# Kernel tuning notes

Measured on AMD Instinct MI355X. Metric: run time of the kernel, lower is better.

The kernel has to match this reference:

```python
import jax, jax.numpy as jnp
import numpy as np

N, E, B, H = 10000, 50000, 512, 64
IN_CH, EDGE_DIM = 11, 4
N_LAYERS, M_STEPS = 4, 3

silu = jax.nn.silu


def setup_inputs() -> dict:
    key = jax.random.key(0)
    ks = jax.random.split(key, 20)
    rn = lambda k, s, sc=0.1: jax.random.normal(k, s, jnp.float32) * sc
    w = 2 * H  # nn_width_factor * hidden
    inp = {
        "x": rn(ks[0], (N, IN_CH), 1.0),
        "edge_attr": jax.random.uniform(ks[1], (E, EDGE_DIM), jnp.float32),
        "pos": rn(ks[2], (N, 3), 1.0),
        "edge_index": jax.random.randint(ks[3], (2, E), 0, N),
        "batch": jnp.sort(jax.random.randint(ks[4], (N,), 0, B)),
        "fl_W": rn(ks[5], (H, IN_CH), 0.3), "fl_b": jnp.zeros(H),
        "nn_W1": rn(ks[6], (w, EDGE_DIM + 1), 0.3), "nn_b1": jnp.zeros(w),
        "nn_W2": rn(ks[7], (H * H, w), 0.02), "nn_b2": jnp.zeros(H * H),
        "root_W": rn(ks[8], (H, H)), "root_b": jnp.zeros(H),
        "gru_Wih": rn(ks[9], (3 * H, H)), "gru_Whh": rn(ks[10], (3 * H, H)),
        "gru_bih": jnp.zeros(3 * H), "gru_bhh": jnp.zeros(3 * H),
        "lstm_Wih": rn(ks[11], (4 * H, 2 * H)), "lstm_Whh": rn(ks[12], (4 * H, H)),
        "lstm_bih": jnp.zeros(4 * H), "lstm_bhh": jnp.zeros(4 * H),
        "out_W1": rn(ks[13], (H, 2 * H)), "out_b1": jnp.zeros(H),
        "out_W2": rn(ks[14], (1, H)), "out_b2": jnp.zeros(1),
    }
    return inp


def _fwd(x, edge_attr, pos, fl_W, fl_b, nn_W1, nn_b1, nn_W2, nn_b2,
         root_W, root_b, gru_Wih, gru_Whh, gru_bih, gru_bhh,
         lstm_Wih, lstm_Whh, lstm_bih, lstm_bhh,
         out_W1, out_b1, out_W2, out_b2, edge_index, batch):
    src, dst = edge_index[0], edge_index[1]
    x = silu(x @ fl_W.T + fl_b)          # [N, H]
    h = x                                 # GRU hidden state

    # Edge-conditioned weights (shared conv + fixed edge_attr/pos -> compute once)
    dist = jnp.linalg.norm(pos[src] - pos[dst], axis=-1, keepdims=True)  # [E,1]
    ef = jnp.concatenate([edge_attr, dist], axis=-1)                      # [E,5]
    W_edge = (silu(ef @ nn_W1.T + nn_b1) @ nn_W2.T + nn_b2).reshape(E, H, H)
    deg = jnp.clip(jax.ops.segment_sum(jnp.ones((E,), x.dtype), dst, num_segments=N), 1.0)[:, None]

    for _ in range(N_LAYERS):
        # NNConv message: x_j @ W(e_ij), mean-aggregated at target i
        m = jnp.einsum('ei,eio->eo', x[src], W_edge)                      # [E, H]
        agg = jax.ops.segment_sum(m, dst, num_segments=N) / deg
        xc = silu(x @ root_W.T + root_b + agg)
        # GRU cell (seq_len=1)
        gi = xc @ gru_Wih.T + gru_bih
        gh = h @ gru_Whh.T + gru_bhh
        i_r, i_z, i_n = jnp.split(gi, 3, axis=-1)
        h_r, h_z, h_n = jnp.split(gh, 3, axis=-1)
        r = jax.nn.sigmoid(i_r + h_r)
        z = jax.nn.sigmoid(i_z + h_z)
        n = jnp.tanh(i_n + r * h_n)
        x = (1.0 - z) * n + z * h
        h = x

    # Set2Set readout (M processing steps, LSTM over graphs)
    q_star = jnp.zeros((B, 2 * H), x.dtype)
    hl = jnp.zeros((B, H), x.dtype)
    cl = jnp.zeros((B, H), x.dtype)
    for _ in range(M_STEPS):
        g = q_star @ lstm_Wih.T + lstm_bih + hl @ lstm_Whh.T + lstm_bhh
        gi_, gf_, gg_, go_ = jnp.split(g, 4, axis=-1)
        cl = jax.nn.sigmoid(gf_) * cl + jax.nn.sigmoid(gi_) * jnp.tanh(gg_)
        hl = jax.nn.sigmoid(go_) * jnp.tanh(cl)
        e = jnp.sum(x * hl[batch], axis=-1)                               # [N]
        mmax = jax.ops.segment_max(e, batch, num_segments=B)
        a = jnp.exp(e - mmax[batch])
        a = a / jax.ops.segment_sum(a, batch, num_segments=B)[batch]
        r_read = jax.ops.segment_sum(a[:, None] * x, batch, num_segments=B)
        q_star = jnp.concatenate([hl, r_read], axis=-1)

    out = silu(q_star @ out_W1.T + out_b1) @ out_W2.T + out_b2            # [B,1]
    return out.squeeze(-1)


def reference(x, edge_index, edge_attr, pos, batch, fl_W, fl_b, nn_W1, nn_b1,
              nn_W2, nn_b2, root_W, root_b, gru_Wih, gru_Whh, gru_bih, gru_bhh,
              lstm_Wih, lstm_Whh, lstm_bih, lstm_bhh, out_W1, out_b1, out_W2, out_b2):
    return _fwd(x, edge_attr, pos, fl_W, fl_b, nn_W1, nn_b1, nn_W2, nn_b2,
                root_W, root_b, gru_Wih, gru_Whh, gru_bih, gru_bhh,
                lstm_Wih, lstm_Whh, lstm_bih, lstm_bhh,
                out_W1, out_b1, out_W2, out_b2, edge_index, batch)
```

## Files before the change

### kernel.cpp

```cpp
#include <hip/hip_runtime.h>
#include <stdint.h>


#define NN 10000
#define EE 50000
#define BBG 512

typedef __attribute__((ext_vector_type(8))) short short8;
typedef __attribute__((ext_vector_type(4))) float f32x4;
typedef __attribute__((ext_vector_type(2))) float f32x2;

__device__ __forceinline__ float b2f(unsigned short u) {
  return __uint_as_float(((unsigned)u) << 16);
}
__device__ __forceinline__ float b2f_lo(unsigned u) { return __uint_as_float(u << 16); }
__device__ __forceinline__ float b2f_hi(unsigned u) { return __uint_as_float(u & 0xFFFF0000u); }
__device__ __forceinline__ unsigned short f2b(float f) {
  unsigned u = __float_as_uint(f);
  u += 0x7FFFu + ((u >> 16) & 1u);
  return (unsigned short)(u >> 16);
}
__device__ __forceinline__ float sigm(float x) { return 1.0f / (1.0f + __expf(-x)); }
__device__ __forceinline__ float siluf(float x) { return x / (1.0f + __expf(-x)); }
__device__ __forceinline__ float rawf(const void* p, int f, int i) {
  return f ? b2f(((const unsigned short*)p)[i]) : ((const float*)p)[i];
}
__device__ __forceinline__ float rdlane(int v, int k) {
  return __int_as_float(__builtin_amdgcn_readlane(v, k));
}

__global__ __launch_bounds__(256) void k_detect(const unsigned* __restrict__ w,
                                                int* __restrict__ flag) {
  __shared__ int cnt;
  if (threadIdx.x == 0) cnt = 0;
  __syncthreads();
  int c = 0;
  for (int i = threadIdx.x; i < 4096; i += 256) {
    unsigned lo = w[i] & 0xFFFFu;
    if (lo - 0x3A00u < 0x600u) c++;
  }
  atomicAdd(&cnt, c);
  __syncthreads();
  if (threadIdx.x == 0) *flag = (cnt > 2048) ? 1 : 0;
}

#define NCVT 20
struct Cvt {
  const void* src[NCVT];
  float* dst[NCVT];
  int n[NCVT];
};

__global__ __launch_bounds__(256) void k_convert(Cvt c, const int* __restrict__ flag) {
  const int f = *flag;
  const int stride = gridDim.x * blockDim.x;
  const int tid = blockIdx.x * blockDim.x + threadIdx.x;
#pragma unroll 1
  for (int a = 0; a < NCVT; a++) {
    const int n = c.n[a];
    const float* sf = (const float*)c.src[a];
    const unsigned short* sb = (const unsigned short*)c.src[a];
    float* d = c.dst[a];
    for (int i = tid; i < n; i += stride) d[i] = f ? b2f(sb[i]) : sf[i];
  }
}

__global__ __launch_bounds__(256) void k_ltrans(const float* __restrict__ Wih,
                                                const float* __restrict__ Whh,
                                                const float* __restrict__ W1,
                                                const float* __restrict__ rW,
                                                const float* __restrict__ gWih,
                                                const float* __restrict__ gWhh,
                                                float* __restrict__ WihT,
                                                float* __restrict__ WhhT,
                                                float* __restrict__ W1T,
                                                float* __restrict__ rWT,
                                                float* __restrict__ gWihT,
                                                float* __restrict__ gWhhT) {
  int j = blockIdx.x * 256 + threadIdx.x;
  if (j < 32768) {
    int r = j & 255, k = j >> 8;
    WihT[k * 256 + r] = Wih[r * 128 + k];
  } else if (j < 49152) {
    int q = j - 32768;
    int r = q & 255, k = q >> 8;
    WhhT[k * 256 + r] = Whh[r * 64 + k];
  } else if (j < 57344) {
    int q = j - 49152;
    int o = q & 63, k = q >> 6;
    W1T[k * 64 + o] = W1[o * 128 + k];
  } else if (j < 61440) {
    int q = j - 57344;
    int o = q & 63, k = q >> 6;
    rWT[k * 64 + o] = rW[o * 64 + k];
  } else if (j < 73728) {
    int q = j - 61440;
    int r = q % 192, k = q / 192;
    gWihT[k * 192 + r] = gWih[r * 64 + k];
  } else if (j < 86016) {
    int q = j - 73728;
    int r = q % 192, k = q / 192;
    gWhhT[k * 192 + r] = gWhh[r * 64 + k];
  }
}

__global__ __launch_bounds__(256) void k_hist(const int* __restrict__ ei,
                                              int* __restrict__ cnt,
                                              int* __restrict__ cntd) {
  int e = blockIdx.x * 256 + threadIdx.x;
  if (e < EE) {
    atomicAdd(cnt + ei[e], 1);
    atomicAdd(cntd + ei[EE + e], 1);
  }
}

__global__ __launch_bounds__(256) void k_scan(const int* __restrict__ cnt,
                                              const int* __restrict__ cntd,
                                              int* __restrict__ eptr,
                                              int* __restrict__ cursor,
                                              float* __restrict__ invd) {
  __shared__ int part[256];
  const int t = threadIdx.x;
  const int c0 = t * 40;
  int s = 0;
  for (int i = 0; i < 40; i++) {
    int idx = c0 + i;
    if (idx < NN) s += cnt[idx];
  }
  part[t] = s;
  __syncthreads();
  if (t == 0) {
    int run = 0;
    for (int i = 0; i < 256; i++) { int v = part[i]; part[i] = run; run += v; }
  }
  __syncthreads();
  int run = part[t];
  for (int i = 0; i < 40; i++) {
    int idx = c0 + i;
    if (idx < NN) {
      eptr[idx] = run;
      cursor[idx] = run;
      run += cnt[idx];
      invd[idx] = 1.0f / fmaxf((float)cntd[idx], 1.0f);
    }
  }
  if (t == 255) eptr[NN] = EE;
}

__global__ __launch_bounds__(256) void k_scatter(const int* __restrict__ ei,
                                                 int* __restrict__ cursor,
                                                 int* __restrict__ eord) {
  int e = blockIdx.x * 256 + threadIdx.x;
  if (e < EE) {
    int pos = atomicAdd(cursor + ei[e], 1);
    eord[pos] = e;
  }
}

__global__ __launch_bounds__(256) void k_sperm(const unsigned short* __restrict__ s_bf,
                                               const int* __restrict__ ei,
                                               const int* __restrict__ eord,
                                               unsigned* __restrict__ s_srt,
                                               int* __restrict__ dst_srt) {
  const int j = blockIdx.x * 4 + (threadIdx.x >> 6);
  const int lane = threadIdx.x & 63;
  const int e = eord[j];
  s_srt[(size_t)j * 64 + lane] = ((const unsigned*)s_bf)[(size_t)e * 64 + lane];
  if (lane == 0) dst_srt[j] = ei[EE + e];
}

__global__ __launch_bounds__(256) void k_lift(const void* __restrict__ xin,
                                              const float* __restrict__ flW,
                                              const float* __restrict__ flb,
                                              const float* __restrict__ b2,
                                              float* __restrict__ x,
                                              unsigned short* __restrict__ xb,
                                              float* __restrict__ xb2,
                                              float* __restrict__ agg,
                                              const int* __restrict__ flag) {
  const int f = *flag;
  int node = blockIdx.x * 4 + (threadIdx.x >> 6);
  int h = threadIdx.x & 63;
  float acc = flb[h];
#pragma unroll
  for (int c = 0; c < 11; c++)
    acc += rawf(xin, f, node * 11 + c) * flW[h * 11 + c];
  float v = siluf(acc);
  x[node * 64 + h] = v;
  xb[node * 64 + h] = f2b(v);
  int xvi = __float_as_int(v);
  float a2 = 0.0f;
#pragma unroll 8
  for (int i = 0; i < 64; i++) {
    float xi = rdlane(xvi, i);
    a2 += xi * b2[i * 64 + h];
  }
  xb2[node * 64 + h] = a2;
  agg[(size_t)node * 64 + h] = 0.0f;
}

__global__ __launch_bounds__(256) void k_sdeg(const void* __restrict__ ea,
                                              const void* __restrict__ pos,
                                              const int* __restrict__ ei,
                                              const float* __restrict__ W1,
                                              const float* __restrict__ b1,
                                              unsigned short* __restrict__ s_bf,
                                              const int* __restrict__ flag) {
  const int f = *flag;
  int e = blockIdx.x * 2 + (threadIdx.x >> 7);
  int k = threadIdx.x & 127;
  int src = ei[e], dst = ei[EE + e];
  float dx = rawf(pos, f, src * 3 + 0) - rawf(pos, f, dst * 3 + 0);
  float dy = rawf(pos, f, src * 3 + 1) - rawf(pos, f, dst * 3 + 1);
  float dz = rawf(pos, f, src * 3 + 2) - rawf(pos, f, dst * 3 + 2);
  float dist = sqrtf(dx * dx + dy * dy + dz * dz);
  float acc = b1[k];
  acc += rawf(ea, f, e * 4 + 0) * W1[k * 5 + 0];
  acc += rawf(ea, f, e * 4 + 1) * W1[k * 5 + 1];
  acc += rawf(ea, f, e * 4 + 2) * W1[k * 5 + 2];
  acc += rawf(ea, f, e * 4 + 3) * W1[k * 5 + 3];
  acc += dist * W1[k * 5 + 4];
  s_bf[e * 128 + k] = f2b(siluf(acc));
}

__global__ __launch_bounds__(256) void k_w2t(const float* __restrict__ W2,
                                             unsigned short* __restrict__ W2t) {
  int j = blockIdx.x * 256 + threadIdx.x;
  int i = j & 63;
  int k = (j >> 6) & 127;
  int o = j >> 13;
  W2t[j] = f2b(W2[(size_t)(i * 64 + o) * 128 + k]);
}

template <int KC>
__global__ __launch_bounds__(256) void k_T(const unsigned short* __restrict__ xb,
                                           const unsigned short* __restrict__ W2t,
                                           unsigned short* __restrict__ Tc, int K0) {
  __shared__ unsigned short sh[2 * 128 * 72];
  unsigned short* As = sh;
  unsigned short* Bs = sh + 128 * 72;
  const int t = threadIdx.x;
  const int n0 = blockIdx.x * 128;
  const int c0 = blockIdx.y * 128;
  const int lane = t & 63;
  const int w = t >> 6;
  const int lm = lane & 15;
  const int quad = lane >> 4;
  const int wm = w & 1;
  const int wn = w >> 1;

  for (int p = t; p < 128 * 8; p += 256) {
    int r = p >> 3, cc = (p & 7) * 8;
    uint4 v = make_uint4(0u, 0u, 0u, 0u);
    if (n0 + r < NN) v = *reinterpret_cast<const uint4*>(xb + (size_t)(n0 + r) * 64 + cc);
    *reinterpret_cast<uint4*>(&As[r * 72 + cc]) = v;
  }
  for (int p = t; p < 128 * 8; p += 256) {
    int r = p >> 3, cc = (p & 7) * 8;
    int c = c0 + r;
    int o = c / KC;
    int kg = K0 + (c % KC);
    uint4 v = *reinterpret_cast<const uint4*>(W2t + (size_t)(o * 128 + kg) * 64 + cc);
    *reinterpret_cast<uint4*>(&Bs[r * 72 + cc]) = v;
  }
  __syncthreads();

  f32x4 acc[4][4];
#pragma unroll
  for (int mt = 0; mt < 4; mt++)
#pragma unroll
    for (int nt = 0; nt < 4; nt++) acc[mt][nt] = (f32x4)(0.0f);

#pragma unroll
  for (int ks = 0; ks < 2; ks++) {
    const int kk = ks * 32 + quad * 8;
    short8 af[4], bfr[4];
#pragma unroll
    for (int mt = 0; mt < 4; mt++)
      af[mt] = *reinterpret_cast<const short8*>(&As[(wm * 64 + mt * 16 + lm) * 72 + kk]);
#pragma unroll
    for (int nt = 0; nt < 4; nt++)
      bfr[nt] = *reinterpret_cast<const short8*>(&Bs[(wn * 64 + nt * 16 + lm) * 72 + kk]);
#pragma unroll
    for (int mt = 0; mt < 4; mt++)
#pragma unroll
      for (int nt = 0; nt < 4; nt++)
        acc[mt][nt] = __builtin_amdgcn_mfma_f32_16x16x32_bf16(af[mt], bfr[nt], acc[mt][nt], 0, 0, 0);
  }

  __syncthreads();
  unsigned short* st = sh;
#pragma unroll
  for (int nt = 0; nt < 4; nt++) {
    int col = wn * 64 + nt * 16 + lm;
#pragma unroll
    for (int mt = 0; mt < 4; mt++) {
#pragma unroll
      for (int reg = 0; reg < 4; reg++) {
        int row = wm * 64 + mt * 16 + quad * 4 + reg;
        st[row * 132 + col] = f2b(acc[mt][nt][reg]);
      }
    }
  }
  __syncthreads();
  const int r16 = t >> 4;
  const int c8 = (t & 15) * 8;
#pragma unroll
  for (int it = 0; it < 8; it++) {
    int row = it * 16 + r16;
    int n = n0 + row;
    if (n < NN) {
      uint2 v0 = *reinterpret_cast<const uint2*>(&st[row * 132 + c8]);
      uint2 v1 = *reinterpret_cast<const uint2*>(&st[row * 132 + c8 + 4]);
      uint4 v = make_uint4(v0.x, v0.y, v1.x, v1.y);
      *reinterpret_cast<uint4*>(Tc + (size_t)n * (64 * KC) + c0 + c8) = v;
    }
  }
}

__global__ __launch_bounds__(256) void k_group(const unsigned short* __restrict__ Tc,
                                               const unsigned* __restrict__ s_srt,
                                               const int* __restrict__ dst_srt,
                                               const float* __restrict__ xb2,
                                               const int* __restrict__ eptr,
                                               float* __restrict__ agg) {
  const int n = blockIdx.x * 4 + (threadIdx.x >> 6);
  const int lane = threadIdx.x & 63;
  const int beg = eptr[n], end = eptr[n + 1];
  if (beg == end) return;
  const int lm = lane & 15;
  const int quad = lane >> 4;

  short8 bf[4][4];
#pragma unroll
  for (int ks = 0; ks < 4; ks++)
#pragma unroll
    for (int ot = 0; ot < 4; ot++)
      bf[ks][ot] = *reinterpret_cast<const short8*>(
          Tc + (size_t)n * 8192 + (ot * 16 + lm) * 128 + ks * 32 + quad * 8);

  float xv[4];
#pragma unroll
  for (int ot = 0; ot < 4; ot++) xv[ot] = xb2[(size_t)n * 64 + ot * 16 + lm];

  for (int tile = beg; tile < end; tile += 16) {
    int eidx = tile + lm;
    if (eidx >= EE) eidx = EE - 1;
    f32x4 acc[4];
#pragma unroll
    for (int ot = 0; ot < 4; ot++) acc[ot] = (f32x4)(0.0f);
#pragma unroll
    for (int ks = 0; ks < 4; ks++) {
      short8 af = *reinterpret_cast<const short8*>(
          (const unsigned short*)s_srt + (size_t)eidx * 128 + ks * 32 + quad * 8);
#pragma unroll
      for (int ot = 0; ot < 4; ot++)
        acc[ot] = __builtin_amdgcn_mfma_f32_16x16x32_bf16(af, bf[ks][ot], acc[ot], 0, 0, 0);
    }
#pragma unroll
    for (int reg = 0; reg < 4; reg++) {
      int edge = tile + quad * 4 + reg;
      if (edge < end) {
        int dst = dst_srt[edge];
#pragma unroll
        for (int ot = 0; ot < 4; ot++)
          atomicAdd(agg + (size_t)dst * 64 + ot * 16 + lm, acc[ot][reg] + xv[ot]);
      }
    }
  }
}

template <int KC>
__global__ __launch_bounds__(256) void k_emsg(const unsigned short* __restrict__ Tc,
                                              const unsigned short* __restrict__ s_bf,
                                              const int* __restrict__ ei,
                                              float* __restrict__ m, int K0, int first) {
  int e = blockIdx.x * 4 + (threadIdx.x >> 6);
  int o = threadIdx.x & 63;
  int src = ei[e];
  const uint4* tv = reinterpret_cast<const uint4*>(Tc + ((size_t)src * 64 + o) * KC);
  const uint4* sv = reinterpret_cast<const uint4*>(s_bf + (size_t)e * 128 + K0);
  float acc = 0.0f;
#pragma unroll
  for (int j = 0; j < KC / 8; j++) {
    uint4 a = tv[j], b = sv[j];
    unsigned aa[4] = {a.x, a.y, a.z, a.w};
    unsigned bb[4] = {b.x, b.y, b.z, b.w};
#pragma unroll
    for (int q = 0; q < 4; q++)
      acc += b2f_lo(aa[q]) * b2f_lo(bb[q]) + b2f_hi(aa[q]) * b2f_hi(bb[q]);
  }
  float* mp = m + (size_t)e * 64 + o;
  if (first) *mp = acc;
  else *mp += acc;
}

__global__ __launch_bounds__(256) void k_aggm(const float* __restrict__ m,
                                              const float* __restrict__ xb2,
                                              const int* __restrict__ ei,
                                              float* __restrict__ agg) {
  int e = blockIdx.x * 4 + (threadIdx.x >> 6);
  int o = threadIdx.x & 63;
  int src = ei[e], dst = ei[EE + e];
  atomicAdd(agg + (size_t)dst * 64 + o, m[(size_t)e * 64 + o] + xb2[(size_t)src * 64 + o]);
}

__global__ __launch_bounds__(256) void k_xcgru(float* __restrict__ x,
                                               unsigned short* __restrict__ xb,
                                               float* __restrict__ agg,
                                               const float* __restrict__ invd,
                                               const float* __restrict__ rWT,
                                               const float* __restrict__ rb,
                                               const float* __restrict__ WihT,
                                               const float* __restrict__ WhhT,
                                               const float* __restrict__ bih,
                                               const float* __restrict__ bhh,
                                               const float* __restrict__ b2,
                                               float* __restrict__ xb2,
                                               int last) {
  const int node0 = (blockIdx.x * 4 + (threadIdx.x >> 6)) * 4;
  const int lane = threadIdx.x & 63;

  float xv[4], av[4], idv[4];
  int xvi[4];
#pragma unroll
  for (int nn = 0; nn < 4; nn++) {
    size_t base = (size_t)(node0 + nn) * 64 + lane;
    xv[nn] = x[base];
    av[nn] = agg[base];
    agg[base] = 0.0f;
    idv[nn] = invd[node0 + nn];
    xvi[nn] = __float_as_int(xv[nn]);
  }

  float acc[4] = {0, 0, 0, 0};
#pragma unroll 8
  for (int k = 0; k < 64; k++) {
    float rw = rWT[k * 64 + lane];
#pragma unroll
    for (int nn = 0; nn < 4; nn++) acc[nn] += rdlane(xvi[nn], k) * rw;
  }
  const float rbv = rb[lane];
  int xci[4];
#pragma unroll
  for (int nn = 0; nn < 4; nn++)
    xci[nn] = __float_as_int(siluf(acc[nn] + rbv + av[nn] * idv[nn]));

  float gi0[4], gi1[4], gi2[4], gh0[4], gh1[4], gh2[4];
  {
    const float bi0 = bih[lane], bi1 = bih[64 + lane], bi2 = bih[128 + lane];
    const float bh0 = bhh[lane], bh1 = bhh[64 + lane], bh2 = bhh[128 + lane];
#pragma unroll
    for (int nn = 0; nn < 4; nn++) {
      gi0[nn] = bi0; gi1[nn] = bi1; gi2[nn] = bi2;
      gh0[nn] = bh0; gh1[nn] = bh1; gh2[nn] = bh2;
    }
  }
#pragma unroll 2
  for (int k = 0; k < 64; k++) {
    const float* wi = WihT + k * 192;
    const float* wh = WhhT + k * 192;
    const float wi0 = wi[lane], wi1 = wi[64 + lane], wi2 = wi[128 + lane];
    const float wh0 = wh[lane], wh1 = wh[64 + lane], wh2 = wh[128 + lane];
#pragma unroll
    for (int nn = 0; nn < 4; nn++) {
      const float xck = rdlane(xci[nn], k);
      const float xvk = rdlane(xvi[nn], k);
      gi0[nn] += xck * wi0; gi1[nn] += xck * wi1; gi2[nn] += xck * wi2;
      gh0[nn] += xvk * wh0; gh1[nn] += xvk * wh1; gh2[nn] += xvk * wh2;
    }
  }

  int xni[4];
#pragma unroll
  for (int nn = 0; nn < 4; nn++) {
    const float r = sigm(gi0[nn] + gh0[nn]);
    const float z = sigm(gi1[nn] + gh1[nn]);
    const float ng = tanhf(gi2[nn] + r * gh2[nn]);
    const float xn = (1.0f - z) * ng + z * xv[nn];
    x[(size_t)(node0 + nn) * 64 + lane] = xn;
    xni[nn] = __float_as_int(xn);
  }

  if (!last) {
#pragma unroll
    for (int nn = 0; nn < 4; nn++)
      xb[(size_t)(node0 + nn) * 64 + lane] = f2b(__int_as_float(xni[nn]));
    float a2[4] = {0, 0, 0, 0};
#pragma unroll 8
    for (int i = 0; i < 64; i++) {
      const float bv = b2[i * 64 + lane];
#pragma unroll
      for (int nn = 0; nn < 4; nn++) a2[nn] += rdlane(xni[nn], i) * bv;
    }
#pragma unroll
    for (int nn = 0; nn < 4; nn++)
      xb2[(size_t)(node0 + nn) * 64 + lane] = a2[nn];
  }
}

__global__ __launch_bounds__(256) void k_s2s(const float* __restrict__ x,
                                             const int* __restrict__ batch,
                                             const float* __restrict__ WihT,
                                             const float* __restrict__ WhhT,
                                             const float* __restrict__ bih,
                                             const float* __restrict__ bhh,
                                             const float* __restrict__ W1T,
                                             const float* __restrict__ b1,
                                             const float* __restrict__ W2,
                                             const float* __restrict__ b2o,
                                             void* __restrict__ out,
                                             const int* __restrict__ flag) {
  const int b = blockIdx.x;
  const int t = threadIdx.x;
  const int lane = t & 63;
  const int w = t >> 6;
  int lo = 0, hi = NN;
  while (lo < hi) { int mid = (lo + hi) >> 1; if (batch[mid] < b) lo = mid + 1; else hi = mid; }
  const int ns = lo;
  hi = NN;
  while (lo < hi) { int mid = (lo + hi) >> 1; if (batch[mid] <= b) lo = mid + 1; else hi = mid; }
  const int cnt = lo - ns;

  __shared__ float hs[64], rs[64], cs[64], gs[256];
  __shared__ float es[512];
  __shared__ float red[4][64];
  __shared__ float wred[4], wsum[4];
  if (t < 64) { hs[t] = 0.0f; rs[t] = 0.0f; cs[t] = 0.0f; }
  __syncthreads();

  for (int step = 0; step < 3; step++) {
    float acc = bih[t] + bhh[t];
#pragma unroll 4
    for (int k = 0; k < 64; k++)
      acc += hs[k] * (WihT[k * 256 + t] + WhhT[k * 256 + t]);
#pragma unroll 4
    for (int k = 0; k < 64; k++)
      acc += rs[k] * WihT[(64 + k) * 256 + t];
    gs[t] = acc;
    __syncthreads();
    if (t < 64) {
      float ig = sigm(gs[t]), fg = sigm(gs[64 + t]);
      float gg = tanhf(gs[128 + t]), og = sigm(gs[192 + t]);
      float c = fg * cs[t] + ig * gg;
      cs[t] = c;
      hs[t] = og * tanhf(c);
    }
    __syncthreads();

    float mxw = -3.4e38f;
    for (int j = w; j < cnt; j += 4) {
      float v = x[(size_t)(ns + j) * 64 + lane] * hs[lane];
#pragma unroll
      for (int mm = 32; mm; mm >>= 1) v += __shfl_xor(v, mm, 64);
      if (lane == 0 && j < 512) es[j] = v;
      mxw = fmaxf(mxw, v);
    }
    if (lane == 0) wred[w] = mxw;
    __syncthreads();
    float mx = fmaxf(fmaxf(wred[0], wred[1]), fmaxf(wred[2], wred[3]));

    float ps = 0.0f;
    for (int i = t; i < cnt && i < 512; i += 256) {
      float a = __expf(es[i] - mx);
      es[i] = a;
      ps += a;
    }
#pragma unroll
    for (int mm = 32; mm; mm >>= 1) ps += __shfl_xor(ps, mm, 64);
    if (lane == 0) wsum[w] = ps;
    __syncthreads();
    float tot = wsum[0] + wsum[1] + wsum[2] + wsum[3];
    float inv = (cnt > 0) ? 1.0f / tot : 0.0f;

    float pr = 0.0f;
    for (int j = w; j < cnt && j < 512; j += 4)
      pr += es[j] * x[(size_t)(ns + j) * 64 + lane];
    red[w][lane] = pr;
    __syncthreads();
    if (t < 64)
      rs[t] = (red[0][t] + red[1][t] + red[2][t] + red[3][t]) * inv;
    __syncthreads();
  }

  if (t < 64) {
    float acc = b1[lane];
#pragma unroll 4
    for (int k = 0; k < 64; k++) acc += hs[k] * W1T[k * 64 + lane];
#pragma unroll 4
    for (int k = 0; k < 64; k++) acc += rs[k] * W1T[(64 + k) * 64 + lane];
    float u = siluf(acc) * W2[lane];
#pragma unroll
    for (int mm = 32; mm; mm >>= 1) u += __shfl_xor(u, mm, 64);
    if (lane == 0) {
      float v = u + b2o[0];
      if (*flag) ((unsigned short*)out)[b] = f2b(v);
      else ((float*)out)[b] = v;
    }
  }
}

template <int KC>
static void run_chunks(const unsigned short* xb, const unsigned short* W2t,
                       unsigned short* Tc, const unsigned short* s_bf,
                       const int* ei, float* m, hipStream_t stream) {
  const int nch = 128 / KC;
  for (int c = 0; c < nch; c++) {
    k_T<KC><<<dim3((NN + 127) / 128, (64 * KC) / 128), 256, 0, stream>>>(xb, W2t, Tc, c * KC);
    k_emsg<KC><<<EE / 4, 256, 0, stream>>>(Tc, s_bf, ei, m, c * KC, c == 0 ? 1 : 0);
  }
}

extern "C" void kernel_launch(void* const* d_in, const int* in_sizes, int n_in,
                              void* d_out, int out_size, void* d_ws, size_t ws_size,
                              hipStream_t stream) {
  (void)n_in; (void)out_size;
  const bool sig_order = (in_sizes[1] == 2 * EE);
  const void* p_x   = d_in[0];
  const void* p_ea  = sig_order ? d_in[2] : d_in[1];
  const void* p_pos = sig_order ? d_in[3] : d_in[2];
  const int* edge_index = (const int*)(sig_order ? d_in[1] : d_in[3]);
  const int* batch      = (const int*)d_in[4];
  const void* p_w[20];
  for (int i = 0; i < 20; i++) p_w[i] = d_in[5 + i];

  char* base = (char*)d_ws;
  size_t off = 0;
  auto alloc = [&](size_t bytes) -> char* {
    char* p = base + off;
    off = (off + bytes + 255) & ~(size_t)255;
    return p;
  };
  int* flag = (int*)alloc(4);
  static const int cvt_n[NCVT] = {
      64 * 11, 64, 128 * 5, 128, 4096 * 128, 4096,
      64 * 64, 64,
      192 * 64, 192 * 64, 192, 192,
      256 * 128, 256 * 64, 256, 256,
      64 * 128, 64, 64, 1};
  float* canon[NCVT];
  for (int i = 0; i < NCVT; i++) canon[i] = (float*)alloc((size_t)cvt_n[i] * 4);
  const float* c_flW  = canon[0];
  const float* c_flb  = canon[1];
  const float* c_W1   = canon[2];
  const float* c_b1   = canon[3];
  const float* c_W2   = canon[4];
  const float* c_b2   = canon[5];
  const float* c_rW   = canon[6];
  const float* c_rb   = canon[7];
  const float* c_gWih = canon[8];
  const float* c_gWhh = canon[9];
  const float* c_gbih = canon[10];
  const float* c_gbhh = canon[11];
  const float* c_lWih = canon[12];
  const float* c_lWhh = canon[13];
  const float* c_lbih = canon[14];
  const float* c_lbhh = canon[15];
  const float* c_oW1  = canon[16];
  const float* c_ob1  = canon[17];
  const float* c_oW2  = canon[18];
  const float* c_ob2  = canon[19];

  unsigned short* s_bf = (unsigned short*)alloc((size_t)EE * 128 * 2);
  unsigned* s_srt = (unsigned*)alloc((size_t)EE * 64 * 4 + 4096);
  int* dst_srt = (int*)alloc((size_t)EE * 4);
  float* m    = (float*)alloc((size_t)EE * 64 * 4);
  float* x    = (float*)alloc((size_t)NN * 64 * 4);
  unsigned short* xb = (unsigned short*)alloc((size_t)NN * 64 * 2);
  float* agg  = (float*)alloc((size_t)NN * 64 * 4);
  float* xb2  = (float*)alloc((size_t)NN * 64 * 4);
  unsigned short* W2t = (unsigned short*)alloc((size_t)4096 * 128 * 2);
  float* invd = (float*)alloc((size_t)NN * 4);
  int* cnt    = (int*)alloc((size_t)2 * NN * 4);
  int* cntd   = cnt + NN;
  int* eptr   = (int*)alloc((size_t)(NN + 1) * 4);
  int* cursor = (int*)alloc((size_t)NN * 4);
  int* eord   = (int*)alloc((size_t)EE * 4);
  float* WihT = (float*)alloc((size_t)128 * 256 * 4);
  float* WhhT = (float*)alloc((size_t)64 * 256 * 4);
  float* W1T  = (float*)alloc((size_t)128 * 64 * 4);
  float* rWT  = (float*)alloc((size_t)64 * 64 * 4);
  float* gWihT = (float*)alloc((size_t)64 * 192 * 4);
  float* gWhhT = (float*)alloc((size_t)64 * 192 * 4);
  size_t base_need = off;

  int KC = 0;
  const int kcs[5] = {128, 64, 32, 16, 8};
  for (int i = 0; i < 5; i++) {
    size_t need = base_need + (size_t)NN * 64 * kcs[i] * 2 + 256;
    if (need <= ws_size) { KC = kcs[i]; break; }
  }
  if (KC == 0) return;
  unsigned short* Tc = (unsigned short*)alloc((size_t)NN * 64 * KC * 2);

  k_detect<<<1, 256, 0, stream>>>((const unsigned*)p_ea, flag);
  Cvt cvt;
  for (int i = 0; i < 20; i++) cvt.src[i] = p_w[i];
  for (int i = 0; i < NCVT; i++) { cvt.dst[i] = canon[i]; cvt.n[i] = cvt_n[i]; }
  k_convert<<<512, 256, 0, stream>>>(cvt, flag);
  k_ltrans<<<336, 256, 0, stream>>>(c_lWih, c_lWhh, c_oW1, c_rW, c_gWih, c_gWhh,
                                    WihT, WhhT, W1T, rWT, gWihT, gWhhT);

  hipMemsetAsync(cnt, 0, (size_t)2 * NN * 4, stream);
  k_lift<<<NN / 4, 256, 0, stream>>>(p_x, c_flW, c_flb, c_b2, x, xb, xb2, agg, flag);
  k_sdeg<<<EE / 2, 256, 0, stream>>>(p_ea, p_pos, edge_index, c_W1, c_b1, s_bf, flag);
  k_w2t<<<(4096 * 128) / 256, 256, 0, stream>>>(c_W2, W2t);
  k_hist<<<(EE + 255) / 256, 256, 0, stream>>>(edge_index, cnt, cntd);
  k_scan<<<1, 256, 0, stream>>>(cnt, cntd, eptr, cursor, invd);
  k_scatter<<<(EE + 255) / 256, 256, 0, stream>>>(edge_index, cursor, eord);
  k_sperm<<<EE / 4, 256, 0, stream>>>(s_bf, edge_index, eord, s_srt, dst_srt);

  for (int layer = 0; layer < 4; layer++) {
    if (KC == 128) {
      k_T<128><<<dim3((NN + 127) / 128, 64), 256, 0, stream>>>(xb, W2t, Tc, 0);
      k_group<<<NN / 4, 256, 0, stream>>>(Tc, s_srt, dst_srt, xb2, eptr, agg);
    } else {
      switch (KC) {
        case 64: run_chunks<64>(xb, W2t, Tc, s_bf, edge_index, m, stream); break;
        case 32: run_chunks<32>(xb, W2t, Tc, s_bf, edge_index, m, stream); break;
        case 16: run_chunks<16>(xb, W2t, Tc, s_bf, edge_index, m, stream); break;
        default: run_chunks<8>(xb, W2t, Tc, s_bf, edge_index, m, stream); break;
      }
      k_aggm<<<EE / 4, 256, 0, stream>>>(m, xb2, edge_index, agg);
    }
    k_xcgru<<<NN / 16, 256, 0, stream>>>(x, xb, agg, invd, rWT, c_rb,
                                         gWihT, gWhhT, c_gbih, c_gbhh,
                                         c_b2, xb2, layer == 3 ? 1 : 0);
  }

  k_s2s<<<BBG, 256, 0, stream>>>(x, batch, WihT, WhhT, c_lbih, c_lbhh,
                                 W1T, c_ob1, c_oW2, c_ob2, d_out, flag);
}
```

Before: 655.3 us.

## Fuse per-node transform GEMM with edge gather-reduce, dropping the Tc buffer

Replaces the two-kernel path (k_T writes a 10000x8192 bf16 Tc tensor to global memory, then k_group reads it back and runs per-edge MFMAs) with one kernel, k_Tg. Each block computes a 128-node by 128-k tile of T for one output channel in shared memory, then walks the source-sorted edges of those nodes. For each edge it does a scalar bf16 dot product over 128 k and atomically adds the result into agg. This removes the large global round-trip of Tc and its allocation. In exchange, each edge's 256-byte s vector is re-read once per output channel (64 times), and MFMA edge math becomes scalar FMAs with one atomic per edge per channel.

Result: slower. 1.169 ms (+78.4%).

```diff
diff --git a/kernel.cpp b/kernel.cpp
--- a/kernel.cpp
+++ b/kernel.cpp
@@ -161,12 +161,16 @@
                                                const int* __restrict__ ei,
                                                const int* __restrict__ eord,
                                                unsigned* __restrict__ s_srt,
+                                               int* __restrict__ src_srt,
                                                int* __restrict__ dst_srt) {
   const int j = blockIdx.x * 4 + (threadIdx.x >> 6);
   const int lane = threadIdx.x & 63;
   const int e = eord[j];
   s_srt[(size_t)j * 64 + lane] = ((const unsigned*)s_bf)[(size_t)e * 64 + lane];
-  if (lane == 0) dst_srt[j] = ei[EE + e];
+  if (lane == 0) {
+    src_srt[j] = ei[e];
+    dst_srt[j] = ei[EE + e];
+  }
 }
 
 __global__ __launch_bounds__(256) void k_lift(const void* __restrict__ xin,
@@ -232,6 +236,106 @@
   W2t[j] = f2b(W2[(size_t)(i * 64 + o) * 128 + k]);
 }
 
+__global__ __launch_bounds__(256) void k_Tg(const unsigned short* __restrict__ xb,
+                                            const unsigned short* __restrict__ W2t,
+                                            const unsigned* __restrict__ s_srt,
+                                            const int* __restrict__ src_srt,
+                                            const int* __restrict__ dst_srt,
+                                            const float* __restrict__ xb2,
+                                            const int* __restrict__ eptr,
+                                            float* __restrict__ agg) {
+  __shared__ unsigned short sh[2 * 128 * 72];
+  unsigned short* As = sh;
+  unsigned short* Bs = sh + 128 * 72;
+  const int t = threadIdx.x;
+  const int n0 = blockIdx.x * 128;
+  const int o = blockIdx.y;
+  const int lane = t & 63;
+  const int w = t >> 6;
+  const int lm = lane & 15;
+  const int quad = lane >> 4;
+  const int wm = w & 1;
+  const int wn = w >> 1;
+
+  for (int p = t; p < 128 * 8; p += 256) {
+    int r = p >> 3, cc = (p & 7) * 8;
+    uint4 v = make_uint4(0u, 0u, 0u, 0u);
+    if (n0 + r < NN) v = *reinterpret_cast<const uint4*>(xb + (size_t)(n0 + r) * 64 + cc);
+    *reinterpret_cast<uint4*>(&As[r * 72 + cc]) = v;
+  }
+  for (int p = t; p < 128 * 8; p += 256) {
+    int r = p >> 3, cc = (p & 7) * 8;
+    uint4 v = *reinterpret_cast<const uint4*>(W2t + (size_t)(o * 128 + r) * 64 + cc);
+    *reinterpret_cast<uint4*>(&Bs[r * 72 + cc]) = v;
+  }
+  __syncthreads();
+
+  f32x4 acc[4][4];
+#pragma unroll
+  for (int mt = 0; mt < 4; mt++)
+#pragma unroll
+    for (int nt = 0; nt < 4; nt++) acc[mt][nt] = (f32x4)(0.0f);
+
+#pragma unroll
+  for (int ks = 0; ks < 2; ks++) {
+    const int kk = ks * 32 + quad * 8;
+    short8 af[4], bfr[4];
+#pragma unroll
+    for (int mt = 0; mt < 4; mt++)
+      af[mt] = *reinterpret_cast<const short8*>(&As[(wm * 64 + mt * 16 + lm) * 72 + kk]);
+#pragma unroll
+    for (int nt = 0; nt < 4; nt++)
+      bfr[nt] = *reinterpret_cast<const short8*>(&Bs[(wn * 64 + nt * 16 + lm) * 72 + kk]);
+#pragma unroll
+    for (int mt = 0; mt < 4; mt++)
+#pragma unroll
+      for (int nt = 0; nt < 4; nt++)
+        acc[mt][nt] = __builtin_amdgcn_mfma_f32_16x16x32_bf16(af[mt], bfr[nt], acc[mt][nt], 0, 0, 0);
+  }
+
+  __syncthreads();
+  unsigned short* st = sh;
+#pragma unroll
+  for (int nt = 0; nt < 4; nt++) {
+    int col = wn * 64 + nt * 16 + lm;
+#pragma unroll
+    for (int mt = 0; mt < 4; mt++) {
+#pragma unroll
+      for (int reg = 0; reg < 4; reg++) {
+        int row = wm * 64 + mt * 16 + quad * 4 + reg;
+        st[row * 136 + col] = f2b(acc[mt][nt][reg]);
+      }
+    }
+  }
+  __syncthreads();
+
+  const int ebeg = eptr[n0];
+  int nend = n0 + 128;
+  if (nend > NN) nend = NN;
+  const int eend = eptr[nend];
+  for (int j = ebeg + t; j < eend; j += 256) {
+    const int srcg = src_srt[j];
+    const uint4* sp = reinterpret_cast<const uint4*>(s_srt + (size_t)j * 64);
+    const uint4* tp = reinterpret_cast<const uint4*>(&st[(srcg - n0) * 136]);
+    float a0 = 0.0f, a1 = 0.0f;
+#pragma unroll
+    for (int q = 0; q < 16; q += 2) {
+      uint4 sv0 = sp[q], tv0 = tp[q];
+      uint4 sv1 = sp[q + 1], tv1 = tp[q + 1];
+      a0 += b2f_lo(sv0.x) * b2f_lo(tv0.x) + b2f_hi(sv0.x) * b2f_hi(tv0.x);
+      a0 += b2f_lo(sv0.y) * b2f_lo(tv0.y) + b2f_hi(sv0.y) * b2f_hi(tv0.y);
+      a0 += b2f_lo(sv0.z) * b2f_lo(tv0.z) + b2f_hi(sv0.z) * b2f_hi(tv0.z);
+      a0 += b2f_lo(sv0.w) * b2f_lo(tv0.w) + b2f_hi(sv0.w) * b2f_hi(tv0.w);
+      a1 += b2f_lo(sv1.x) * b2f_lo(tv1.x) + b2f_hi(sv1.x) * b2f_hi(tv1.x);
+      a1 += b2f_lo(sv1.y) * b2f_lo(tv1.y) + b2f_hi(sv1.y) * b2f_hi(tv1.y);
+      a1 += b2f_lo(sv1.z) * b2f_lo(tv1.z) + b2f_hi(sv1.z) * b2f_hi(tv1.z);
+      a1 += b2f_lo(sv1.w) * b2f_lo(tv1.w) + b2f_hi(sv1.w) * b2f_hi(tv1.w);
+    }
+    atomicAdd(agg + (size_t)dst_srt[j] * 64 + o,
+              a0 + a1 + xb2[(size_t)srcg * 64 + o]);
+  }
+}
+
 template <int KC>
 __global__ __launch_bounds__(256) void k_T(const unsigned short* __restrict__ xb,
                                            const unsigned short* __restrict__ W2t,
@@ -314,58 +418,6 @@
       uint2 v1 = *reinterpret_cast<const uint2*>(&st[row * 132 + c8 + 4]);
       uint4 v = make_uint4(v0.x, v0.y, v1.x, v1.y);
       *reinterpret_cast<uint4*>(Tc + (size_t)n * (64 * KC) + c0 + c8) = v;
-    }
-  }
-}
-
-__global__ __launch_bounds__(256) void k_group(const unsigned short* __restrict__ Tc,
-                                               const unsigned* __restrict__ s_srt,
-                                               const int* __restrict__ dst_srt,
-                                               const float* __restrict__ xb2,
-                                               const int* __restrict__ eptr,
-                                               float* __restrict__ agg) {
-  const int n = blockIdx.x * 4 + (threadIdx.x >> 6);
-  const int lane = threadIdx.x & 63;
-  const int beg = eptr[n], end = eptr[n + 1];
-  if (beg == end) return;
-  const int lm = lane & 15;
-  const int quad = lane >> 4;
-
-  short8 bf[4][4];
-#pragma unroll
-  for (int ks = 0; ks < 4; ks++)
-#pragma unroll
-    for (int ot = 0; ot < 4; ot++)
-      bf[ks][ot] = *reinterpret_cast<const short8*>(
-          Tc + (size_t)n * 8192 + (ot * 16 + lm) * 128 + ks * 32 + quad * 8);
-
-  float xv[4];
-#pragma unroll
-  for (int ot = 0; ot < 4; ot++) xv[ot] = xb2[(size_t)n * 64 + ot * 16 + lm];
-
-  for (int tile = beg; tile < end; tile += 16) {
-    int eidx = tile + lm;
-    if (eidx >= EE) eidx = EE - 1;
-    f32x4 acc[4];
-#pragma unroll
-    for (int ot = 0; ot < 4; ot++) acc[ot] = (f32x4)(0.0f);
-#pragma unroll
-    for (int ks = 0; ks < 4; ks++) {
-      short8 af = *reinterpret_cast<const short8*>(
-          (const unsigned short*)s_srt + (size_t)eidx * 128 + ks * 32 + quad * 8);
-#pragma unroll
-      for (int ot = 0; ot < 4; ot++)
-        acc[ot] = __builtin_amdgcn_mfma_f32_16x16x32_bf16(af, bf[ks][ot], acc[ot], 0, 0, 0);
-    }
-#pragma unroll
-    for (int reg = 0; reg < 4; reg++) {
-      int edge = tile + quad * 4 + reg;
-      if (edge < end) {
-        int dst = dst_srt[edge];
-#pragma unroll
-        for (int ot = 0; ot < 4; ot++)
-          atomicAdd(agg + (size_t)dst * 64 + ot * 16 + lm, acc[ot][reg] + xv[ot]);
-      }
     }
   }
 }
@@ -663,6 +715,7 @@
 
   unsigned short* s_bf = (unsigned short*)alloc((size_t)EE * 128 * 2);
   unsigned* s_srt = (unsigned*)alloc((size_t)EE * 64 * 4 + 4096);
+  int* src_srt = (int*)alloc((size_t)EE * 4);
   int* dst_srt = (int*)alloc((size_t)EE * 4);
   float* m    = (float*)alloc((size_t)EE * 64 * 4);
   float* x    = (float*)alloc((size_t)NN * 64 * 4);
@@ -685,13 +738,17 @@
   size_t base_need = off;
 
   int KC = 0;
-  const int kcs[5] = {128, 64, 32, 16, 8};
-  for (int i = 0; i < 5; i++) {
-    size_t need = base_need + (size_t)NN * 64 * kcs[i] * 2 + 256;
-    if (need <= ws_size) { KC = kcs[i]; break; }
+  if (base_need <= ws_size) KC = 128;
+  else {
+    const int kcs[4] = {64, 32, 16, 8};
+    for (int i = 0; i < 4; i++) {
+      size_t need = base_need + (size_t)NN * 64 * kcs[i] * 2 + 256;
+      if (need <= ws_size) { KC = kcs[i]; break; }
+    }
   }
   if (KC == 0) return;
-  unsigned short* Tc = (unsigned short*)alloc((size_t)NN * 64 * KC * 2);
+  unsigned short* Tc = nullptr;
+  if (KC < 128) Tc = (unsigned short*)alloc((size_t)NN * 64 * KC * 2);
 
   k_detect<<<1, 256, 0, stream>>>((const unsigned*)p_ea, flag);
   Cvt cvt;
@@ -708,12 +765,12 @@
   k_hist<<<(EE + 255) / 256, 256, 0, stream>>>(edge_index, cnt, cntd);
   k_scan<<<1, 256, 0, stream>>>(cnt, cntd, eptr, cursor, invd);
   k_scatter<<<(EE + 255) / 256, 256, 0, stream>>>(edge_index, cursor, eord);
-  k_sperm<<<EE / 4, 256, 0, stream>>>(s_bf, edge_index, eord, s_srt, dst_srt);
+  k_sperm<<<EE / 4, 256, 0, stream>>>(s_bf, edge_index, eord, s_srt, src_srt, dst_srt);
 
   for (int layer = 0; layer < 4; layer++) {
     if (KC == 128) {
-      k_T<128><<<dim3((NN + 127) / 128, 64), 256, 0, stream>>>(xb, W2t, Tc, 0);
-      k_group<<<NN / 4, 256, 0, stream>>>(Tc, s_srt, dst_srt, xb2, eptr, agg);
+      k_Tg<<<dim3((NN + 127) / 128, 64), 256, 0, stream>>>(
+          xb, W2t, s_srt, src_srt, dst_srt, xb2, eptr, agg);
     } else {
       switch (KC) {
         case 64: run_chunks<64>(xb, W2t, Tc, s_bf, edge_index, m, stream); break;
```
